# Optimization experiments

Measured on AMD Instinct MI355X. Metric: run time of the kernel, lower is better.

The kernel has to match this reference:

```python
import jax, jax.numpy as jnp
import numpy as np

N_NODES = 100000
N_EDGES = 6400000
IN_CH, HID, OUT_CH = 128, 16, 32


def setup_inputs() -> dict:
    key = jax.random.key(0)
    k1, k2, k3, k4 = jax.random.split(key, 4)
    x = jax.random.normal(k1, (N_NODES, IN_CH), dtype=jnp.float32)
    edge_index = jax.random.randint(k2, (2, N_EDGES), 0, N_NODES, dtype=jnp.int64)
    # glorot-ish scaled weights
    W1 = jax.random.normal(k3, (IN_CH, HID), dtype=jnp.float32) * (1.0 / np.sqrt(IN_CH))
    W2 = jax.random.normal(k4, (HID, OUT_CH), dtype=jnp.float32) * (1.0 / np.sqrt(HID))
    b1 = jnp.zeros((HID,), dtype=jnp.float32)
    b2 = jnp.zeros((OUT_CH,), dtype=jnp.float32)
    return {"x": x, "edge_index": edge_index, "W1": W1, "b1": b1, "W2": W2, "b2": b2}


def reference(x, edge_index, W1, b1, W2, b2):
    N = x.shape[0]
    # PyG GCNConv: add self-loops, symmetric D^{-1/2} A D^{-1/2} normalization
    loop = jnp.arange(N, dtype=edge_index.dtype)
    src = jnp.concatenate([edge_index[0], loop])  # [E+N]
    dst = jnp.concatenate([edge_index[1], loop])  # [E+N]
    deg = jax.ops.segment_sum(jnp.ones_like(dst, dtype=x.dtype), dst, num_segments=N)
    deg_inv_sqrt = jnp.where(deg > 0, jax.lax.rsqrt(deg), 0.0)
    norm = deg_inv_sqrt[src] * deg_inv_sqrt[dst]  # [E+N]

    def gcn_conv(h, W, b):
        h = h @ W                                   # transform first (small out dim)
        msg = h[src] * norm[:, None]                # gather + scale
        agg = jax.ops.segment_sum(msg, dst, num_segments=N)  # scatter-add
        return agg + b

    h = jax.nn.relu(gcn_conv(x, W1, b1))
    return gcn_conv(h, W2, b2)
```

## Files before the change

kernel.cpp:

```cpp
#include <hip/hip_runtime.h>


#define IN_CH 128
#define HID 16
#define OUT_CH 32

#define TILE 8192
#define BSHIFT 8
#define BNODES 256
#define BCAP 17408
#define NBUCK_MAX 512

typedef __attribute__((ext_vector_type(4))) _Float16 half4;

__global__ __launch_bounds__(512) void bucket_kernel(
    const int* __restrict__ src, const int* __restrict__ dst,
    int* __restrict__ bcur, int* __restrict__ bpacked, int E, int nbuck) {
  __shared__ int stage[TILE];
  __shared__ unsigned char stg_b[TILE];
  __shared__ int hist[NBUCK_MAX];
  __shared__ int scn[NBUCK_MAX];
  __shared__ int cur[NBUCK_MAX];
  __shared__ int gbase[NBUCK_MAX];

  int tid = threadIdx.x;
  int base = blockIdx.x * TILE;
  int cnt_t = E - base; if (cnt_t > TILE) cnt_t = TILE;
  bool full = (cnt_t == TILE);

  hist[tid] = 0;
  __syncthreads();

  int4 d4[4], s4[4];
  if (full) {
    const int4* dv = (const int4*)(dst + base);
    #pragma unroll
    for (int k = 0; k < 4; ++k) d4[k] = dv[tid + 512 * k];
    #pragma unroll
    for (int k = 0; k < 4; ++k) {
      atomicAdd(&hist[d4[k].x >> BSHIFT], 1);
      atomicAdd(&hist[d4[k].y >> BSHIFT], 1);
      atomicAdd(&hist[d4[k].z >> BSHIFT], 1);
      atomicAdd(&hist[d4[k].w >> BSHIFT], 1);
    }
    const int4* sv = (const int4*)(src + base);
    #pragma unroll
    for (int k = 0; k < 4; ++k) s4[k] = sv[tid + 512 * k];
  } else {
    for (int i = tid; i < cnt_t; i += 512)
      atomicAdd(&hist[dst[base + i] >> BSHIFT], 1);
  }
  __syncthreads();
  scn[tid] = hist[tid];
  __syncthreads();
  for (int off = 1; off < 512; off <<= 1) {
    int a0 = (tid >= off) ? scn[tid - off] : 0;
    __syncthreads();
    scn[tid] += a0;
    __syncthreads();
  }
  {
    int b = tid;
    int excl = scn[b] - hist[b];
    cur[b] = excl;
    int c = hist[b];
    gbase[b] = (b < nbuck && c > 0) ? atomicAdd(&bcur[b], c) : 0;
  }
  __syncthreads();
  if (full) {
    #pragma unroll
    for (int k = 0; k < 4; ++k) {
      int dd[4] = {d4[k].x, d4[k].y, d4[k].z, d4[k].w};
      int ss[4] = {s4[k].x, s4[k].y, s4[k].z, s4[k].w};
      #pragma unroll
      for (int c = 0; c < 4; ++c) {
        int d = dd[c], s = ss[c];
        int b = d >> BSHIFT;
        int r = atomicAdd(&cur[b], 1);
        stage[r] = ((b >> 8) << 25) | ((d & 255) << 17) | s;
        stg_b[r] = (unsigned char)b;
      }
    }
  } else {
    for (int i = tid; i < cnt_t; i += 512) {
      int d = dst[base + i];
      int s = src[base + i];
      int b = d >> BSHIFT;
      int r = atomicAdd(&cur[b], 1);
      stage[r] = ((b >> 8) << 25) | ((d & 255) << 17) | s;
      stg_b[r] = (unsigned char)b;
    }
  }
  __syncthreads();
  for (int i = tid; i < cnt_t; i += 512) {
    int sv = stage[i];
    int b = stg_b[i] | (((sv >> 25) & 1) << 8);
    int excl = scn[b] - hist[b];
    int pos = gbase[b] + (i - excl);
    if (pos < BCAP) bpacked[(size_t)b * BCAP + pos] = sv & 0x1FFFFFF;
  }
}

__global__ __launch_bounds__(1024) void nodesort_kernel(
    const int* __restrict__ bpacked, const int* __restrict__ bcur,
    int* __restrict__ csr, int* __restrict__ row_ptr, int* __restrict__ cnt,
    float* __restrict__ dis, int N) {
  __shared__ int h[BNODES];
  __shared__ int sc[BNODES];
  __shared__ int cu[BNODES];
  int b = blockIdx.x;
  int tid = threadIdx.x;
  if (tid < BNODES) h[tid] = 0;
  __syncthreads();
  int ecnt = bcur[b]; if (ecnt > BCAP) ecnt = BCAP;
  int ecnt4 = ecnt & ~3;
  const int* bp = bpacked + (size_t)b * BCAP;
  for (int i4 = tid; i4 * 4 < ecnt4; i4 += 1024) {
    int4 p = ((const int4*)bp)[i4];
    atomicAdd(&h[(p.x >> 17) & 255], 1);
    atomicAdd(&h[(p.y >> 17) & 255], 1);
    atomicAdd(&h[(p.z >> 17) & 255], 1);
    atomicAdd(&h[(p.w >> 17) & 255], 1);
  }
  if (ecnt4 + tid < ecnt) atomicAdd(&h[(bp[ecnt4 + tid] >> 17) & 255], 1);
  __syncthreads();
  if (tid < BNODES) sc[tid] = h[tid];
  __syncthreads();
  for (int off = 1; off < BNODES; off <<= 1) {
    int t = 0;
    if (tid < BNODES && tid >= off) t = sc[tid - off];
    __syncthreads();
    if (tid < BNODES) sc[tid] += t;
    __syncthreads();
  }
  if (tid < BNODES) cu[tid] = sc[tid] - h[tid];
  __syncthreads();
  int* cb = csr + (size_t)b * BCAP;
  for (int i4 = tid; i4 * 4 < ecnt4; i4 += 1024) {
    int4 p = ((const int4*)bp)[i4];
    int r;
    r = atomicAdd(&cu[(p.x >> 17) & 255], 1); cb[r] = p.x & 0x1FFFF;
    r = atomicAdd(&cu[(p.y >> 17) & 255], 1); cb[r] = p.y & 0x1FFFF;
    r = atomicAdd(&cu[(p.z >> 17) & 255], 1); cb[r] = p.z & 0x1FFFF;
    r = atomicAdd(&cu[(p.w >> 17) & 255], 1); cb[r] = p.w & 0x1FFFF;
  }
  if (ecnt4 + tid < ecnt) {
    int p = bp[ecnt4 + tid];
    int r = atomicAdd(&cu[(p >> 17) & 255], 1);
    cb[r] = p & 0x1FFFF;
  }
  if (tid < BNODES) {
    int node = (b << BSHIFT) + tid;
    if (node < N) {
      row_ptr[node] = b * BCAP + (sc[tid] - h[tid]);
      cnt[node] = h[tid];
      dis[node] = rsqrtf((float)h[tid] + 1.0f);
    }
  }
}

__global__ __launch_bounds__(256) void gemm1_kernel(
    const float* __restrict__ x, const float* __restrict__ W1,
    const float* __restrict__ dis, _Float16* __restrict__ t1h, int N) {
  __shared__ __align__(16) float xs[64 * 132];
  __shared__ __align__(16) float w1s[128 * 16];
  int tid = threadIdx.x;
  int nb = blockIdx.x * 64;
  for (int i = tid; i < 128 * 16; i += 256) w1s[i] = W1[i];
  int maxRows = N - nb; if (maxRows > 64) maxRows = 64;
  const float4* xg = (const float4*)(x + (size_t)nb * IN_CH);
  for (int i = tid; i < maxRows * 32; i += 256) {
    float4 v = xg[i];
    int row = i >> 5;
    int k4 = (i & 31) << 2;
    *((float4*)&xs[row * 132 + k4]) = v;
  }
  __syncthreads();
  int nl = tid >> 2;
  int cg = tid & 3;
  int node = nb + nl;
  float4 acc = make_float4(0.f, 0.f, 0.f, 0.f);
  const float* xrow = &xs[nl * 132];
  const float4* w4 = (const float4*)w1s;
  for (int k = 0; k < 128; ++k) {
    float xv = xrow[k];
    float4 wv = w4[k * 4 + cg];
    acc.x += xv * wv.x; acc.y += xv * wv.y;
    acc.z += xv * wv.z; acc.w += xv * wv.w;
  }
  if (node < N) {
    float dd = dis[node];
    half4 hv;
    hv.x = (_Float16)(acc.x * dd);
    hv.y = (_Float16)(acc.y * dd);
    hv.z = (_Float16)(acc.z * dd);
    hv.w = (_Float16)(acc.w * dd);
    *((half4*)&t1h[(size_t)node * HID + cg * 4]) = hv;
  }
}

template <bool RELU>
__global__ __launch_bounds__(256) void ggather_kernel(
    const int* __restrict__ row_ptr, const int* __restrict__ cnt,
    const int* __restrict__ csr, const float* __restrict__ dis,
    const _Float16* __restrict__ feat, const float* __restrict__ bias,
    const float* __restrict__ W2, const float* __restrict__ b2,
    _Float16* __restrict__ out16, float* __restrict__ outp, int N) {
  __shared__ __align__(16) float w2s[16 * 32];
  __shared__ __align__(16) float b2s[32];
  int tid = threadIdx.x;
  if (!RELU) {
    for (int i = tid; i < 16 * 32; i += 256) w2s[i] = W2[i];
    if (tid < 32) b2s[tid] = b2[tid];
    __syncthreads();
  }
  int gid = blockIdx.x * 256 + tid;
  int node = gid >> 3;
  if (node >= N) return;
  int half = (gid >> 2) & 1;
  int q4 = (gid & 3) << 2;
  int beg = row_ptr[node];
  int c = cnt[node];
  const int* row = csr + beg;
  half4 sf = *(const half4*)(feat + (size_t)node * HID + q4);
  float dd = dis[node];
  float ax = 0.f, ay = 0.f, az = 0.f, aw = 0.f;
  int j = half;
  for (; j + 30 < c; j += 32) {
    int s[16];
    #pragma unroll
    for (int e = 0; e < 16; ++e) s[e] = row[j + 2 * e];
    half4 f[16];
    #pragma unroll
    for (int e = 0; e < 16; ++e)
      f[e] = *(const half4*)(feat + (size_t)s[e] * HID + q4);
    #pragma unroll
    for (int e = 0; e < 16; ++e) {
      ax += (float)f[e].x; ay += (float)f[e].y;
      az += (float)f[e].z; aw += (float)f[e].w;
    }
  }
  for (; j + 14 < c; j += 16) {
    int s[8];
    #pragma unroll
    for (int e = 0; e < 8; ++e) s[e] = row[j + 2 * e];
    half4 f[8];
    #pragma unroll
    for (int e = 0; e < 8; ++e)
      f[e] = *(const half4*)(feat + (size_t)s[e] * HID + q4);
    #pragma unroll
    for (int e = 0; e < 8; ++e) {
      ax += (float)f[e].x; ay += (float)f[e].y;
      az += (float)f[e].z; aw += (float)f[e].w;
    }
  }
  for (; j < c; j += 2) {
    int s = row[j];
    half4 f = *(const half4*)(feat + (size_t)s * HID + q4);
    ax += (float)f.x; ay += (float)f.y; az += (float)f.z; aw += (float)f.w;
  }
  ax += __shfl_down(ax, 4);
  ay += __shfl_down(ay, 4);
  az += __shfl_down(az, 4);
  aw += __shfl_down(aw, 4);
  if (RELU) {
    if (half == 0) {
      float rx = dd * (ax + (float)sf.x);
      float ry = dd * (ay + (float)sf.y);
      float rz = dd * (az + (float)sf.z);
      float rw = dd * (aw + (float)sf.w);
      float4 bb = *(const float4*)(bias + q4);
      rx = fmaxf(rx + bb.x, 0.f) * dd;
      ry = fmaxf(ry + bb.y, 0.f) * dd;
      rz = fmaxf(rz + bb.z, 0.f) * dd;
      rw = fmaxf(rw + bb.w, 0.f) * dd;
      half4 hv;
      hv.x = (_Float16)rx; hv.y = (_Float16)ry;
      hv.z = (_Float16)rz; hv.w = (_Float16)rw;
      *((half4*)&out16[(size_t)node * HID + q4]) = hv;
    }
  } else {
    float rv0 = dd * (ax + (float)sf.x);
    float rv1 = dd * (ay + (float)sf.y);
    float rv2 = dd * (az + (float)sf.z);
    float rv3 = dd * (aw + (float)sf.w);
    int lane = tid & 63;
    int laneBase = lane & ~7;
    int k = lane & 7;
    float4 acc = ((const float4*)b2s)[k];
    #pragma unroll
    for (int q = 0; q < 4; ++q) {
      float c0 = __shfl(rv0, laneBase + q);
      float c1 = __shfl(rv1, laneBase + q);
      float c2 = __shfl(rv2, laneBase + q);
      float c3 = __shfl(rv3, laneBase + q);
      float4 w0 = ((const float4*)&w2s[(4 * q + 0) * 32])[k];
      float4 w1 = ((const float4*)&w2s[(4 * q + 1) * 32])[k];
      float4 w2v = ((const float4*)&w2s[(4 * q + 2) * 32])[k];
      float4 w3 = ((const float4*)&w2s[(4 * q + 3) * 32])[k];
      acc.x += c0 * w0.x + c1 * w1.x + c2 * w2v.x + c3 * w3.x;
      acc.y += c0 * w0.y + c1 * w1.y + c2 * w2v.y + c3 * w3.y;
      acc.z += c0 * w0.z + c1 * w1.z + c2 * w2v.z + c3 * w3.z;
      acc.w += c0 * w0.w + c1 * w1.w + c2 * w2v.w + c3 * w3.w;
    }
    *((float4*)&outp[(size_t)node * OUT_CH + (size_t)k * 4]) = acc;
  }
}

extern "C" void kernel_launch(void* const* d_in, const int* in_sizes, int n_in,
                              void* d_out, int out_size, void* d_ws, size_t ws_size,
                              hipStream_t stream) {
  const float* x  = (const float*)d_in[0];
  const int* ei   = (const int*)d_in[1];
  const float* W1 = (const float*)d_in[2];
  const float* b1 = (const float*)d_in[3];
  const float* W2 = (const float*)d_in[4];
  const float* b2 = (const float*)d_in[5];
  float* out = (float*)d_out;

  int N = in_sizes[0] / IN_CH;
  int E = in_sizes[1] / 2;
  const int* src = ei;
  const int* dst = ei + E;

  int nbuck = (N + BNODES - 1) >> BSHIFT;

  int*      bcur    = (int*)d_ws;
  float*    dis     = (float*)(bcur + 512);
  int*      row_ptr = (int*)(dis + N);
  int*      cnt     = row_ptr + N;
  _Float16* t1h     = (_Float16*)(cnt + N);
  _Float16* h1h     = t1h + (size_t)N * HID;
  int*      bpacked = (int*)(h1h + (size_t)N * HID);
  int*      csr     = bpacked + (size_t)nbuck * BCAP;

  hipMemsetAsync(bcur, 0, 512 * sizeof(int), stream);

  bucket_kernel<<<(E + TILE - 1) / TILE, 512, 0, stream>>>(
      src, dst, bcur, bpacked, E, nbuck);
  nodesort_kernel<<<nbuck, 1024, 0, stream>>>(
      bpacked, bcur, csr, row_ptr, cnt, dis, N);
  gemm1_kernel<<<(N + 63) / 64, 256, 0, stream>>>(x, W1, dis, t1h, N);
  ggather_kernel<true><<<((size_t)N * 8 + 255) / 256, 256, 0, stream>>>(
      row_ptr, cnt, csr, dis, t1h, b1, nullptr, nullptr, h1h, nullptr, N);
  ggather_kernel<false><<<((size_t)N * 8 + 255) / 256, 256, 0, stream>>>(
      row_ptr, cnt, csr, dis, h1h, nullptr, W2, b2, nullptr, out, N);
}
```

Before: 290.8 us.

## Use 16 threads per node in gather and register-cache bucket entries in nodesort

The gather kernels now assign 16 threads per node, four edge partitions times four feature quads, instead of 8. A second shuffle stage reduces the partial sums, and the W2 epilogue is remapped so each lane writes two output columns. Nodesort loads each thread's bucket entries into registers once, up to 5 int4 loads, and reuses them for both the histogram and the scatter, removing the second global read. The extra gather parallelism targets latency hiding on the ~64-edge rows but doubles thread count and shrinks per-thread unrolling.

```diff
diff --git a/kernel.cpp b/kernel.cpp
--- a/kernel.cpp
+++ b/kernel.cpp
@@ -115,14 +115,30 @@
   int ecnt = bcur[b]; if (ecnt > BCAP) ecnt = BCAP;
   int ecnt4 = ecnt & ~3;
   const int* bp = bpacked + (size_t)b * BCAP;
-  for (int i4 = tid; i4 * 4 < ecnt4; i4 += 1024) {
-    int4 p = ((const int4*)bp)[i4];
-    atomicAdd(&h[(p.x >> 17) & 255], 1);
-    atomicAdd(&h[(p.y >> 17) & 255], 1);
-    atomicAdd(&h[(p.z >> 17) & 255], 1);
-    atomicAdd(&h[(p.w >> 17) & 255], 1);
-  }
-  if (ecnt4 + tid < ecnt) atomicAdd(&h[(bp[ecnt4 + tid] >> 17) & 255], 1);
+  const int4* bp4 = (const int4*)bp;
+
+  int4 p[5];
+  bool g[5];
+  #pragma unroll
+  for (int k = 0; k < 5; ++k) {
+    int i4 = tid + k * 1024;
+    g[k] = (i4 * 4 < ecnt4);
+    if (g[k]) p[k] = bp4[i4];
+  }
+  int tl = 0;
+  bool gt = (ecnt4 + tid < ecnt);
+  if (gt) tl = bp[ecnt4 + tid];
+
+  #pragma unroll
+  for (int k = 0; k < 5; ++k) {
+    if (g[k]) {
+      atomicAdd(&h[(p[k].x >> 17) & 255], 1);
+      atomicAdd(&h[(p[k].y >> 17) & 255], 1);
+      atomicAdd(&h[(p[k].z >> 17) & 255], 1);
+      atomicAdd(&h[(p[k].w >> 17) & 255], 1);
+    }
+  }
+  if (gt) atomicAdd(&h[(tl >> 17) & 255], 1);
   __syncthreads();
   if (tid < BNODES) sc[tid] = h[tid];
   __syncthreads();
@@ -136,18 +152,19 @@
   if (tid < BNODES) cu[tid] = sc[tid] - h[tid];
   __syncthreads();
   int* cb = csr + (size_t)b * BCAP;
-  for (int i4 = tid; i4 * 4 < ecnt4; i4 += 1024) {
-    int4 p = ((const int4*)bp)[i4];
-    int r;
-    r = atomicAdd(&cu[(p.x >> 17) & 255], 1); cb[r] = p.x & 0x1FFFF;
-    r = atomicAdd(&cu[(p.y >> 17) & 255], 1); cb[r] = p.y & 0x1FFFF;
-    r = atomicAdd(&cu[(p.z >> 17) & 255], 1); cb[r] = p.z & 0x1FFFF;
-    r = atomicAdd(&cu[(p.w >> 17) & 255], 1); cb[r] = p.w & 0x1FFFF;
-  }
-  if (ecnt4 + tid < ecnt) {
-    int p = bp[ecnt4 + tid];
-    int r = atomicAdd(&cu[(p >> 17) & 255], 1);
-    cb[r] = p & 0x1FFFF;
+  #pragma unroll
+  for (int k = 0; k < 5; ++k) {
+    if (g[k]) {
+      int r;
+      r = atomicAdd(&cu[(p[k].x >> 17) & 255], 1); cb[r] = p[k].x & 0x1FFFF;
+      r = atomicAdd(&cu[(p[k].y >> 17) & 255], 1); cb[r] = p[k].y & 0x1FFFF;
+      r = atomicAdd(&cu[(p[k].z >> 17) & 255], 1); cb[r] = p[k].z & 0x1FFFF;
+      r = atomicAdd(&cu[(p[k].w >> 17) & 255], 1); cb[r] = p[k].w & 0x1FFFF;
+    }
+  }
+  if (gt) {
+    int r = atomicAdd(&cu[(tl >> 17) & 255], 1);
+    cb[r] = tl & 0x1FFFF;
   }
   if (tid < BNODES) {
     int node = (b << BSHIFT) + tid;
@@ -215,35 +232,22 @@
     __syncthreads();
   }
   int gid = blockIdx.x * 256 + tid;
-  int node = gid >> 3;
+  int node = gid >> 4;
   if (node >= N) return;
-  int half = (gid >> 2) & 1;
-  int q4 = (gid & 3) << 2;
+  int sub = gid & 15;
+  int par = sub >> 2;
+  int q4 = (sub & 3) << 2;
   int beg = row_ptr[node];
   int c = cnt[node];
   const int* row = csr + beg;
   half4 sf = *(const half4*)(feat + (size_t)node * HID + q4);
   float dd = dis[node];
   float ax = 0.f, ay = 0.f, az = 0.f, aw = 0.f;
-  int j = half;
-  for (; j + 30 < c; j += 32) {
-    int s[16];
-    #pragma unroll
-    for (int e = 0; e < 16; ++e) s[e] = row[j + 2 * e];
-    half4 f[16];
-    #pragma unroll
-    for (int e = 0; e < 16; ++e)
-      f[e] = *(const half4*)(feat + (size_t)s[e] * HID + q4);
-    #pragma unroll
-    for (int e = 0; e < 16; ++e) {
-      ax += (float)f[e].x; ay += (float)f[e].y;
-      az += (float)f[e].z; aw += (float)f[e].w;
-    }
-  }
-  for (; j + 14 < c; j += 16) {
+  int j = par;
+  for (; j + 28 < c; j += 32) {
     int s[8];
     #pragma unroll
-    for (int e = 0; e < 8; ++e) s[e] = row[j + 2 * e];
+    for (int e = 0; e < 8; ++e) s[e] = row[j + 4 * e];
     half4 f[8];
     #pragma unroll
     for (int e = 0; e < 8; ++e)
@@ -254,17 +258,17 @@
       az += (float)f[e].z; aw += (float)f[e].w;
     }
   }
-  for (; j < c; j += 2) {
+  for (; j < c; j += 4) {
     int s = row[j];
     half4 f = *(const half4*)(feat + (size_t)s * HID + q4);
     ax += (float)f.x; ay += (float)f.y; az += (float)f.z; aw += (float)f.w;
   }
-  ax += __shfl_down(ax, 4);
-  ay += __shfl_down(ay, 4);
-  az += __shfl_down(az, 4);
-  aw += __shfl_down(aw, 4);
+  ax += __shfl_down(ax, 4); ax += __shfl_down(ax, 8);
+  ay += __shfl_down(ay, 4); ay += __shfl_down(ay, 8);
+  az += __shfl_down(az, 4); az += __shfl_down(az, 8);
+  aw += __shfl_down(aw, 4); aw += __shfl_down(aw, 8);
   if (RELU) {
-    if (half == 0) {
+    if (sub < 4) {
       float rx = dd * (ax + (float)sf.x);
       float ry = dd * (ay + (float)sf.y);
       float rz = dd * (az + (float)sf.z);
@@ -285,25 +289,24 @@
     float rv2 = dd * (az + (float)sf.z);
     float rv3 = dd * (aw + (float)sf.w);
     int lane = tid & 63;
-    int laneBase = lane & ~7;
-    int k = lane & 7;
-    float4 acc = ((const float4*)b2s)[k];
+    int base16 = lane & ~15;
+    int k = lane & 15;
+    float a0 = b2s[2 * k], a1 = b2s[2 * k + 1];
     #pragma unroll
     for (int q = 0; q < 4; ++q) {
-      float c0 = __shfl(rv0, laneBase + q);
-      float c1 = __shfl(rv1, laneBase + q);
-      float c2 = __shfl(rv2, laneBase + q);
-      float c3 = __shfl(rv3, laneBase + q);
-      float4 w0 = ((const float4*)&w2s[(4 * q + 0) * 32])[k];
-      float4 w1 = ((const float4*)&w2s[(4 * q + 1) * 32])[k];
-      float4 w2v = ((const float4*)&w2s[(4 * q + 2) * 32])[k];
-      float4 w3 = ((const float4*)&w2s[(4 * q + 3) * 32])[k];
-      acc.x += c0 * w0.x + c1 * w1.x + c2 * w2v.x + c3 * w3.x;
-      acc.y += c0 * w0.y + c1 * w1.y + c2 * w2v.y + c3 * w3.y;
-      acc.z += c0 * w0.z + c1 * w1.z + c2 * w2v.z + c3 * w3.z;
-      acc.w += c0 * w0.w + c1 * w1.w + c2 * w2v.w + c3 * w3.w;
-    }
-    *((float4*)&outp[(size_t)node * OUT_CH + (size_t)k * 4]) = acc;
+      float c0 = __shfl(rv0, base16 + q);
+      float c1 = __shfl(rv1, base16 + q);
+      float c2 = __shfl(rv2, base16 + q);
+      float c3 = __shfl(rv3, base16 + q);
+      const float* w0 = &w2s[(4 * q + 0) * 32 + 2 * k];
+      const float* w1 = &w2s[(4 * q + 1) * 32 + 2 * k];
+      const float* w2p = &w2s[(4 * q + 2) * 32 + 2 * k];
+      const float* w3 = &w2s[(4 * q + 3) * 32 + 2 * k];
+      a0 += c0 * w0[0] + c1 * w1[0] + c2 * w2p[0] + c3 * w3[0];
+      a1 += c0 * w0[1] + c1 * w1[1] + c2 * w2p[1] + c3 * w3[1];
+    }
+    float2 r2; r2.x = a0; r2.y = a1;
+    *((float2*)&outp[(size_t)node * OUT_CH + 2 * k]) = r2;
   }
 }
 
@@ -341,8 +344,8 @@
   nodesort_kernel<<<nbuck, 1024, 0, stream>>>(
       bpacked, bcur, csr, row_ptr, cnt, dis, N);
   gemm1_kernel<<<(N + 63) / 64, 256, 0, stream>>>(x, W1, dis, t1h, N);
-  ggather_kernel<true><<<((size_t)N * 8 + 255) / 256, 256, 0, stream>>>(
+  ggather_kernel<true><<<((size_t)N * 16 + 255) / 256, 256, 0, stream>>>(
       row_ptr, cnt, csr, dis, t1h, b1, nullptr, nullptr, h1h, nullptr, N);
-  ggather_kernel<false><<<((size_t)N * 8 + 255) / 256, 256, 0, stream>>>(
+  ggather_kernel<false><<<((size_t)N * 16 + 255) / 256, 256, 0, stream>>>(
       row_ptr, cnt, csr, dis, h1h, nullptr, W2, b2, nullptr, out, N);
 }
```

Measured after the change: 284.2 us. 1.02x faster.
